# Performance work log

Hardware: AMD Instinct MI355X
Metric: run time of the kernel (lower is better)

The kernel has to match this reference:

```python
import jax, jax.numpy as jnp
import numpy as np

HEADS = 8
DIM_HEAD = 64
C = 512              # in_channels == inner_dim = heads*dim_head
WIN = 7              # window size implied by rel_pos table (2*7-1 = 13)
EPS = 1e-5


def setup_inputs() -> dict:
    key = jax.random.key(0)
    ks = jax.random.split(key, 6)
    B = 2048
    inner = HEADS * DIM_HEAD
    x = jax.random.normal(ks[0], (B, C, WIN, WIN), dtype=jnp.float32)
    gamma = jnp.ones((C,), dtype=jnp.float32)
    beta = jnp.zeros((C,), dtype=jnp.float32)
    w_qkv = jax.random.normal(ks[1], (C, 3 * inner), dtype=jnp.float32) / np.sqrt(C)
    rel_table = jax.random.normal(ks[2], (2 * WIN - 1, 2 * WIN - 1, HEADS), dtype=jnp.float32)
    w_out = jax.random.normal(ks[3], (inner, C), dtype=jnp.float32) / np.sqrt(inner)
    b_out = jnp.zeros((C,), dtype=jnp.float32)
    return {"x": x, "gamma": gamma, "beta": beta, "w_qkv": w_qkv,
            "rel_table": rel_table, "w_out": w_out, "b_out": b_out}


def _rel_pos_bias(rel_table, H, W):
    # Swin-style additive bias: bias[h, i, j] = table[hi-hj+H-1, wi-wj+W-1, h]
    hh = jnp.arange(H)
    ww = jnp.arange(W)
    hi = jnp.repeat(hh, W)          # [N] row index of each flattened position
    wi = jnp.tile(ww, H)            # [N] col index
    dh = hi[:, None] - hi[None, :] + (H - 1)   # [N, N]
    dw = wi[:, None] - wi[None, :] + (W - 1)   # [N, N]
    bias = rel_table[dh, dw]        # [N, N, heads]
    return jnp.transpose(bias, (2, 0, 1))      # [heads, N, N]


def reference(x, gamma, beta, w_qkv, rel_table, w_out, b_out):
    B, Cc, H, W = x.shape
    N = H * W
    shortcut = x
    xs = jnp.transpose(x.reshape(B, Cc, N), (0, 2, 1))   # [B, N, C]
    # LayerNorm over channel dim
    mu = jnp.mean(xs, axis=-1, keepdims=True)
    var = jnp.var(xs, axis=-1, keepdims=True)
    xn = (xs - mu) * jax.lax.rsqrt(var + EPS) * gamma + beta
    qkv = xn @ w_qkv                                      # [B, N, 3*inner]
    q, k, v = jnp.split(qkv, 3, axis=-1)
    def heads(t):
        return jnp.transpose(t.reshape(B, N, HEADS, DIM_HEAD), (0, 2, 1, 3))  # [B,h,N,d]
    q, k, v = heads(q), heads(k), heads(v)
    scale = DIM_HEAD ** -0.5
    dots = jnp.einsum('bhnd,bhmd->bhnm', q, k) * scale   # [B,h,N,N]
    dots = dots + _rel_pos_bias(rel_table, H, W)[None]   # add Swin-style bias
    attn = jax.nn.softmax(dots, axis=-1)
    out = jnp.einsum('bhnm,bhmd->bhnd', attn, v)         # [B,h,N,d]
    out = jnp.transpose(out, (0, 2, 1, 3)).reshape(B, N, HEADS * DIM_HEAD)
    out = out @ w_out + b_out                            # [B, N, C]
    out = jnp.transpose(out, (0, 2, 1)).reshape(B, Cc, H, W)
    return out + shortcut
```

## Files before the change

kernel.cpp:

```cpp
#include <hip/hip_runtime.h>

#define BATCH 2048
#define CH 512
#define NTOK 49
#define NHEAD 8
#define DHEAD 64

typedef __attribute__((ext_vector_type(8))) short bf16x8;
typedef __attribute__((ext_vector_type(4))) float f32x4;

__device__ __forceinline__ ushort f2bf(float f) {
  union { float f; unsigned u; } v; v.f = f;
  unsigned r = v.u + 0x7fffu + ((v.u >> 16) & 1u);
  return (ushort)(r >> 16);
}

__device__ __forceinline__ float bf2f(ushort u) {
  union { unsigned u; float f; } v; v.u = ((unsigned)u) << 16;
  return v.f;
}

#define MFMA16(a, b, c) __builtin_amdgcn_mfma_f32_16x16x32_bf16((a), (b), (c), 0, 0, 0)

#define GLOAD_LDS16(gsrc, ldst)                                                  \
  __builtin_amdgcn_global_load_lds((const __attribute__((address_space(1))) void*)(gsrc), \
                                   (__attribute__((address_space(3))) void*)(ldst), 16, 0, 0)

__global__ void prep_kernel(const float* __restrict__ w_qkv, const float* __restrict__ w_out,
                            const float* __restrict__ rel, ushort* __restrict__ wqkvB,
                            ushort* __restrict__ woutF, float* __restrict__ biasP) {
  int tid = blockIdx.x * blockDim.x + threadIdx.x;
  int stride = gridDim.x * blockDim.x;
  for (int i = tid; i < 12 * 16 * 8 * 64 * 8; i += stride) {
    int j = i & 7, lane = (i >> 3) & 63, cbs = (i >> 9) & 7, kk = (i >> 12) & 15, nb = i >> 16;
    int o = nb * 128 + cbs * 16 + (lane & 15);
    int c = kk * 32 + (lane >> 4) * 8 + j;
    wqkvB[i] = f2bf(w_qkv[c * 1536 + o]);
  }
  for (int i = tid; i < 32 * 16 * 64 * 8; i += stride) {
    int j = i & 7, lane = (i >> 3) & 63, ks = (i >> 9) & 15, cb = i >> 13;
    int o = cb * 16 + (lane & 15);
    int c = ks * 32 + (lane >> 4) * 8 + j;
    woutF[i] = f2bf(w_out[c * 512 + o]);
  }
  for (int i = tid; i < NHEAD * 64 * 64; i += stride) {
    int h = i >> 12, n = (i >> 6) & 63, m = i & 63;
    float v = -1e30f;
    if (n < NTOK && m < NTOK) {
      int dh = n / 7 - m / 7 + 6;
      int dw = n % 7 - m % 7 + 6;
      v = rel[(dh * 13 + dw) * 8 + h];
    }
    biasP[i] = v;
  }
}

__global__ __launch_bounds__(256) void ln_kernel(const float* __restrict__ x,
                                                 const float* __restrict__ gamma,
                                                 const float* __restrict__ beta,
                                                 ushort* __restrict__ xnW) {
  int b = blockIdx.x;
  int t = threadIdx.x;
  __shared__ ushort xsb[CH][NTOK];
  __shared__ float muL[64], rsL[64];
  const float4* x4 = (const float4*)(x + (size_t)b * CH * NTOK);
  for (int i4 = t; i4 < CH * NTOK / 4; i4 += 256) {
    float4 v = x4[i4];
    int lf = i4 * 4;
#pragma unroll
    for (int e = 0; e < 4; e++) {
      int idx = lf + e;
      int c = idx / NTOK, n = idx - c * NTOK;
      xsb[c][n] = f2bf(((const float*)&v)[e]);
    }
  }
  __syncthreads();
  int row = t >> 2, sub = t & 3;
  float s = 0.f, s2 = 0.f;
  if (row < NTOK) {
    for (int c = sub; c < CH; c += 4) {
      float v = bf2f(xsb[c][row]);
      s += v;
      s2 += v * v;
    }
  }
  s += __shfl_xor(s, 1);
  s += __shfl_xor(s, 2);
  s2 += __shfl_xor(s2, 1);
  s2 += __shfl_xor(s2, 2);
  if (sub == 0 && row < NTOK) {
    float m = s * (1.f / CH);
    muL[row] = m;
    rsL[row] = rsqrtf(s2 * (1.f / CH) - m * m + 1e-5f);
  }
  __syncthreads();
  ushort* dst = xnW + (size_t)b * NTOK * CH;
  for (int i = t; i < NTOK * 64; i += 256) {
    int n = i >> 6, c0 = (i & 63) * 8;
    float mu = muL[n], rs = rsL[n];
    ushort tmp[8];
#pragma unroll
    for (int j = 0; j < 8; j++) {
      int c = c0 + j;
      tmp[j] = f2bf((bf2f(xsb[c][n]) - mu) * rs * gamma[c] + beta[c]);
    }
    *(uint4*)(dst + (size_t)n * CH + c0) = *(const uint4*)tmp;
  }
}

__global__ __launch_bounds__(256, 4) void qkv_gemm(const ushort* __restrict__ xnW,
                                                   const ushort* __restrict__ wqkvB,
                                                   ushort* __restrict__ qW,
                                                   ushort* __restrict__ kW,
                                                   ushort* __restrict__ vW) {
  int bid = blockIdx.x;
  int f = (bid & 7) * 1176 + (bid >> 3);
  int mb = f / 12, nb = f - mb * 12;
  int r0 = mb * 128;
  int t = threadIdx.x, lane = t & 63, w = t >> 6;
  int wm = w >> 1, wn = w & 1;

  __shared__ __align__(16) ushort lds[16384];

  const int arow = lane & 15, g = lane >> 4;
  const ushort* wBbase = wqkvB + (size_t)nb * 16 * 4096;
  const ushort* xbase = xnW + (size_t)r0 * CH;

  int drow = t >> 3;
  int slot = t & 7;
  int gchunk = slot ^ (drow & 7);

#pragma unroll
  for (int i = 0; i < 4; i++) {
    int row = drow + i * 32;
    GLOAD_LDS16(xbase + (size_t)row * CH + gchunk * 8, lds + i * 2048 + t * 8);
  }
  __syncthreads();

  f32x4 acc[4][4];
#pragma unroll
  for (int mt = 0; mt < 4; mt++)
#pragma unroll
    for (int nt = 0; nt < 4; nt++) acc[mt][nt] = (f32x4){0.f, 0.f, 0.f, 0.f};

  int cur = 0;
  for (int stage = 0; stage < 8; ++stage) {
    if (stage < 7) {
      int nxt = cur ^ 1, kk = stage + 1;
#pragma unroll
      for (int i = 0; i < 4; i++) {
        GLOAD_LDS16(xbase + (size_t)(drow + i * 32) * CH + kk * 64 + gchunk * 8,
                    lds + nxt * 8192 + i * 2048 + t * 8);
      }
    }
    const ushort* lA = lds + cur * 8192;
#pragma unroll
    for (int ks = 0; ks < 2; ks++) {
      int kk2 = stage * 2 + ks;
      const ushort* wp = wBbase + (size_t)kk2 * 4096 + (wn * 4) * 512 + lane * 8;
      bf16x8 bfr[4];
#pragma unroll
      for (int nt = 0; nt < 4; nt++) bfr[nt] = *(const bf16x8*)(wp + nt * 512);
      bf16x8 afr[4];
#pragma unroll
      for (int mt = 0; mt < 4; mt++) {
        int row = wm * 64 + mt * 16 + arow;
        afr[mt] = *(const bf16x8*)&lA[row * 64 + ((ks * 4 + g) ^ (arow & 7)) * 8];
      }
#pragma unroll
      for (int mt = 0; mt < 4; mt++)
#pragma unroll
        for (int nt = 0; nt < 4; nt++) acc[mt][nt] = MFMA16(afr[mt], bfr[nt], acc[mt][nt]);
    }
    __syncthreads();
    cur ^= 1;
  }

  ushort(*oL)[136] = (ushort(*)[136])lds;
  int h0 = (nb & 3) * 2;
  int sct = nb >> 2;
#pragma unroll
  for (int hh = 0; hh < 2; hh++) {
    if (wm == hh) {
#pragma unroll
      for (int mt = 0; mt < 4; mt++)
#pragma unroll
        for (int nt = 0; nt < 4; nt++)
#pragma unroll
          for (int r = 0; r < 4; r++) {
            int rn = mt * 16 + 4 * g + r;
            oL[rn][wn * 64 + nt * 16 + arow] = f2bf(acc[mt][nt][r]);
          }
    }
    __syncthreads();
    if (sct < 2) {
      ushort* dst = (sct == 0 ? qW : kW);
      for (int i = t; i < 64 * 16; i += 256) {
        int rn = i >> 4, c8 = i & 15;
        int grow = r0 + hh * 64 + rn;
        int b = grow / 49, n = grow - b * 49;
        int h = h0 + (c8 >> 3);
        *(uint4*)(dst + (size_t)(b * 8 + h) * (NTOK * 64) + n * 64 + (c8 & 7) * 8) =
            *(const uint4*)&oL[rn][c8 * 8];
      }
    } else {
      for (int i = t; i < 64 * 128; i += 256) {
        int rn = i & 63, col = i >> 6;
        int grow = r0 + hh * 64 + rn;
        int b = grow / 49, n = grow - b * 49;
        int h = h0 + (col >> 6), d = col & 63;
        vW[(size_t)(b * 8 + h) * 4096 + d * 64 + n] = oL[rn][col];
      }
    }
    __syncthreads();
  }
}

__global__ __launch_bounds__(512) void attnproj(const ushort* __restrict__ qW,
                                                const ushort* __restrict__ kW,
                                                const ushort* __restrict__ vW,
                                                const float* __restrict__ biasP,
                                                const ushort* __restrict__ woutF,
                                                const float* __restrict__ b_out,
                                                const float* __restrict__ x,
                                                float* __restrict__ out) {
  int b = blockIdx.x;
  int t = threadIdx.x;
  int lane = t & 63;
  int w = t >> 6;

  __shared__ __align__(16) ushort lds[36864];
  ushort(*pl)[72] = (ushort(*)[72])(lds + w * 4608);

  const int c = lane & 15, g = lane >> 4;
  const ushort* qb = qW + (size_t)(b * 8 + w) * NTOK * 64;
  const ushort* kb = kW + (size_t)(b * 8 + w) * NTOK * 64;
  const ushort* vb = vW + (size_t)(b * 8 + w) * 64 * 64;
  const float* bp = biasP + w * 64 * 64;

  f32x4 s[4][4];
#pragma unroll
  for (int mt = 0; mt < 4; mt++)
#pragma unroll
    for (int nt = 0; nt < 4; nt++) s[mt][nt] = (f32x4){0.f, 0.f, 0.f, 0.f};
#pragma unroll
  for (int ks = 0; ks < 2; ks++) {
    bf16x8 kf[4];
#pragma unroll
    for (int nt = 0; nt < 4; nt++)
      kf[nt] = *(const bf16x8*)(kb + (size_t)(nt * 16 + c) * 64 + ks * 32 + g * 8);
#pragma unroll
    for (int mt = 0; mt < 4; mt++) {
      bf16x8 qf = *(const bf16x8*)(qb + (size_t)(mt * 16 + c) * 64 + ks * 32 + g * 8);
#pragma unroll
      for (int nt = 0; nt < 4; nt++) s[mt][nt] = MFMA16(qf, kf[nt], s[mt][nt]);
    }
  }
#pragma unroll
  for (int mt = 0; mt < 4; mt++)
#pragma unroll
    for (int nt = 0; nt < 4; nt++)
#pragma unroll
      for (int r = 0; r < 4; r++) {
        int n = mt * 16 + 4 * g + r;
        int m = nt * 16 + c;
        s[mt][nt][r] = s[mt][nt][r] * 0.125f + bp[n * 64 + m];
      }

#pragma unroll
  for (int mt = 0; mt < 4; mt++)
#pragma unroll
    for (int r = 0; r < 4; r++) {
      float mx = fmaxf(fmaxf(s[mt][0][r], s[mt][1][r]), fmaxf(s[mt][2][r], s[mt][3][r]));
      mx = fmaxf(mx, __shfl_xor(mx, 1));
      mx = fmaxf(mx, __shfl_xor(mx, 2));
      mx = fmaxf(mx, __shfl_xor(mx, 4));
      mx = fmaxf(mx, __shfl_xor(mx, 8));
      float p0 = __expf(s[mt][0][r] - mx);
      float p1 = __expf(s[mt][1][r] - mx);
      float p2 = __expf(s[mt][2][r] - mx);
      float p3 = __expf(s[mt][3][r] - mx);
      float sum = p0 + p1 + p2 + p3;
      sum += __shfl_xor(sum, 1);
      sum += __shfl_xor(sum, 2);
      sum += __shfl_xor(sum, 4);
      sum += __shfl_xor(sum, 8);
      float rinv = 1.f / sum;
      int n = mt * 16 + 4 * g + r;
      pl[n][0 * 16 + c] = f2bf(p0 * rinv);
      pl[n][1 * 16 + c] = f2bf(p1 * rinv);
      pl[n][2 * 16 + c] = f2bf(p2 * rinv);
      pl[n][3 * 16 + c] = f2bf(p3 * rinv);
    }

  f32x4 o[4][4];
#pragma unroll
  for (int mt = 0; mt < 4; mt++)
#pragma unroll
    for (int nt = 0; nt < 4; nt++) o[mt][nt] = (f32x4){0.f, 0.f, 0.f, 0.f};
#pragma unroll
  for (int ks = 0; ks < 2; ks++) {
    bf16x8 vf[4];
#pragma unroll
    for (int nt = 0; nt < 4; nt++)
      vf[nt] = *(const bf16x8*)(vb + (size_t)(nt * 16 + c) * 64 + ks * 32 + g * 8);
#pragma unroll
    for (int mt = 0; mt < 4; mt++) {
      bf16x8 pf = *(const bf16x8*)&pl[mt * 16 + c][ks * 32 + g * 8];
#pragma unroll
      for (int nt = 0; nt < 4; nt++) o[mt][nt] = MFMA16(pf, vf[nt], o[mt][nt]);
    }
  }
  __syncthreads();

  ushort(*aoL)[520] = (ushort(*)[520])lds;
#pragma unroll
  for (int mt = 0; mt < 4; mt++)
#pragma unroll
    for (int nt = 0; nt < 4; nt++)
#pragma unroll
      for (int r = 0; r < 4; r++) {
        int n = mt * 16 + 4 * g + r;
        aoL[n][w * 64 + nt * 16 + c] = (n < NTOK) ? f2bf(o[mt][nt][r]) : (ushort)0;
      }
  __syncthreads();

  f32x4 pacc[4][4];
#pragma unroll
  for (int mt = 0; mt < 4; mt++)
#pragma unroll
    for (int nt = 0; nt < 4; nt++) pacc[mt][nt] = (f32x4){0.f, 0.f, 0.f, 0.f};
#pragma unroll 4
  for (int step = 0; step < 16; step++) {
    bf16x8 bfr[4];
#pragma unroll
    for (int nt = 0; nt < 4; nt++)
      bfr[nt] = *(const bf16x8*)(woutF + ((size_t)((w * 4 + nt) * 16 + step)) * 512 + lane * 8);
    bf16x8 afr[4];
#pragma unroll
    for (int mt = 0; mt < 4; mt++)
      afr[mt] = *(const bf16x8*)&aoL[mt * 16 + c][step * 32 + g * 8];
#pragma unroll
    for (int mt = 0; mt < 4; mt++)
#pragma unroll
      for (int nt = 0; nt < 4; nt++) pacc[mt][nt] = MFMA16(afr[mt], bfr[nt], pacc[mt][nt]);
  }

  float(*oL)[260] = (float(*)[260])lds;
  for (int half = 0; half < 2; half++) {
    __syncthreads();
    if ((w >> 2) == half) {
      int wl = w & 3;
#pragma unroll
      for (int mt = 0; mt < 4; mt++)
#pragma unroll
        for (int nt = 0; nt < 4; nt++)
#pragma unroll
          for (int r = 0; r < 4; r++) {
            int rn = mt * 16 + 4 * g + r;
            if (rn < NTOK) oL[rn][wl * 64 + nt * 16 + c] = pacc[mt][nt][r];
          }
    }
    __syncthreads();
    int c0 = half * 256;
    const float4* x4 = (const float4*)(x + ((size_t)b * CH + c0) * NTOK);
    float4* o4 = (float4*)(out + ((size_t)b * CH + c0) * NTOK);
    const float* bo = b_out + c0;
    for (int i = t; i < 3136; i += 512) {
      float4 xv = x4[i];
      float4 ov;
      int lf = i * 4;
#pragma unroll
      for (int e = 0; e < 4; e++) {
        int cl = (lf + e) / NTOK, n = (lf + e) - cl * NTOK;
        ((float*)&ov)[e] = oL[n][cl] + bo[cl] + ((const float*)&xv)[e];
      }
      o4[i] = ov;
    }
  }
}

extern "C" void kernel_launch(void* const* d_in, const int* in_sizes, int n_in,
                              void* d_out, int out_size, void* d_ws, size_t ws_size,
                              hipStream_t stream) {
  const float* x = (const float*)d_in[0];
  const float* gamma = (const float*)d_in[1];
  const float* beta = (const float*)d_in[2];
  const float* w_qkv = (const float*)d_in[3];
  const float* rel = (const float*)d_in[4];
  const float* w_out = (const float*)d_in[5];
  const float* b_out = (const float*)d_in[6];
  float* out = (float*)d_out;

  char* ws = (char*)d_ws;
  size_t off = 0;
  ushort* wqkvB = (ushort*)(ws + off); off += (size_t)12 * 16 * 4096 * 2;
  ushort* woutF = (ushort*)(ws + off); off += (size_t)512 * 512 * 2;
  float* biasP = (float*)(ws + off);   off += (size_t)NHEAD * 64 * 64 * 4;
  ushort* qW = (ushort*)(ws + off);    off += ((size_t)BATCH * 8 * NTOK * 64 + 1024) * 2;
  ushort* kW = (ushort*)(ws + off);    off += ((size_t)BATCH * 8 * NTOK * 64 + 1024) * 2;
  ushort* vW = (ushort*)(ws + off);    off += (size_t)BATCH * 8 * 64 * 64 * 2;
  ushort* xnW = (ushort*)(ws + off);   off += (size_t)BATCH * NTOK * CH * 2;
  (void)ws_size;

  prep_kernel<<<1024, 256, 0, stream>>>(w_qkv, w_out, rel, wqkvB, woutF, biasP);
  ln_kernel<<<BATCH, 256, 0, stream>>>(x, gamma, beta, xnW);
  qkv_gemm<<<784 * 12, 256, 0, stream>>>(xnW, wqkvB, qW, kW, vW);
  attnproj<<<BATCH, 512, 0, stream>>>(qW, kW, vW, biasP, woutF, b_out, x, out);
}
```

Before: 589.2 us.

## Prelayout attention bias per lane, fold q scale into QKV GEMM, prefetch w_out fragments

Result: faster. 560.3 us (-4.9%).

```diff
diff --git a/kernel.cpp b/kernel.cpp
--- a/kernel.cpp
+++ b/kernel.cpp
@@ -28,7 +28,7 @@
 
 __global__ void prep_kernel(const float* __restrict__ w_qkv, const float* __restrict__ w_out,
                             const float* __restrict__ rel, ushort* __restrict__ wqkvB,
-                            ushort* __restrict__ woutF, float* __restrict__ biasP) {
+                            ushort* __restrict__ woutF, float* __restrict__ biasF) {
   int tid = blockIdx.x * blockDim.x + threadIdx.x;
   int stride = gridDim.x * blockDim.x;
   for (int i = tid; i < 12 * 16 * 8 * 64 * 8; i += stride) {
@@ -43,15 +43,23 @@
     int c = ks * 32 + (lane >> 4) * 8 + j;
     woutF[i] = f2bf(w_out[c * 512 + o]);
   }
-  for (int i = tid; i < NHEAD * 64 * 64; i += stride) {
-    int h = i >> 12, n = (i >> 6) & 63, m = i & 63;
-    float v = -1e30f;
-    if (n < NTOK && m < NTOK) {
-      int dh = n / 7 - m / 7 + 6;
-      int dw = n % 7 - m % 7 + 6;
-      v = rel[(dh * 13 + dw) * 8 + h];
-    }
-    biasP[i] = v;
+  for (int i = tid; i < NHEAD * 4 * 4 * 64; i += stride) {
+    int lane = i & 63, nt = (i >> 6) & 3, mt = (i >> 8) & 3, h = i >> 10;
+    int cc = lane & 15, g = lane >> 4;
+    float4 v;
+#pragma unroll
+    for (int r = 0; r < 4; r++) {
+      int n = mt * 16 + 4 * g + r;
+      int m = nt * 16 + cc;
+      float bv = -1e30f;
+      if (n < NTOK && m < NTOK) {
+        int dh = n / 7 - m / 7 + 6;
+        int dw = n % 7 - m % 7 + 6;
+        bv = rel[(dh * 13 + dw) * 8 + h];
+      }
+      ((float*)&v)[r] = bv;
+    }
+    ((float4*)biasF)[i] = v;
   }
 }
 
@@ -179,6 +187,7 @@
   ushort(*oL)[136] = (ushort(*)[136])lds;
   int h0 = (nb & 3) * 2;
   int sct = nb >> 2;
+  float sc = (sct == 0) ? 0.125f : 1.0f;
 #pragma unroll
   for (int hh = 0; hh < 2; hh++) {
     if (wm == hh) {
@@ -189,7 +198,7 @@
 #pragma unroll
           for (int r = 0; r < 4; r++) {
             int rn = mt * 16 + 4 * g + r;
-            oL[rn][wn * 64 + nt * 16 + arow] = f2bf(acc[mt][nt][r]);
+            oL[rn][wn * 64 + nt * 16 + arow] = f2bf(acc[mt][nt][r] * sc);
           }
     }
     __syncthreads();
@@ -219,7 +228,7 @@
 __global__ __launch_bounds__(512) void attnproj(const ushort* __restrict__ qW,
                                                 const ushort* __restrict__ kW,
                                                 const ushort* __restrict__ vW,
-                                                const float* __restrict__ biasP,
+                                                const float* __restrict__ biasF,
                                                 const ushort* __restrict__ woutF,
                                                 const float* __restrict__ b_out,
                                                 const float* __restrict__ x,
@@ -236,13 +245,14 @@
   const ushort* qb = qW + (size_t)(b * 8 + w) * NTOK * 64;
   const ushort* kb = kW + (size_t)(b * 8 + w) * NTOK * 64;
   const ushort* vb = vW + (size_t)(b * 8 + w) * 64 * 64;
-  const float* bp = biasP + w * 64 * 64;
+  const float4* bf = (const float4*)biasF + (size_t)w * 16 * 64;
 
   f32x4 s[4][4];
 #pragma unroll
   for (int mt = 0; mt < 4; mt++)
 #pragma unroll
     for (int nt = 0; nt < 4; nt++) s[mt][nt] = (f32x4){0.f, 0.f, 0.f, 0.f};
+  __builtin_amdgcn_s_setprio(1);
 #pragma unroll
   for (int ks = 0; ks < 2; ks++) {
     bf16x8 kf[4];
@@ -256,16 +266,16 @@
       for (int nt = 0; nt < 4; nt++) s[mt][nt] = MFMA16(qf, kf[nt], s[mt][nt]);
     }
   }
-#pragma unroll
-  for (int mt = 0; mt < 4; mt++)
-#pragma unroll
-    for (int nt = 0; nt < 4; nt++)
-#pragma unroll
-      for (int r = 0; r < 4; r++) {
-        int n = mt * 16 + 4 * g + r;
-        int m = nt * 16 + c;
-        s[mt][nt][r] = s[mt][nt][r] * 0.125f + bp[n * 64 + m];
-      }
+  __builtin_amdgcn_s_setprio(0);
+
+#pragma unroll
+  for (int mt = 0; mt < 4; mt++)
+#pragma unroll
+    for (int nt = 0; nt < 4; nt++) {
+      float4 bb = bf[(mt * 4 + nt) * 64 + lane];
+#pragma unroll
+      for (int r = 0; r < 4; r++) s[mt][nt][r] += ((const float*)&bb)[r];
+    }
 
 #pragma unroll
   for (int mt = 0; mt < 4; mt++)
@@ -298,6 +308,7 @@
   for (int mt = 0; mt < 4; mt++)
 #pragma unroll
     for (int nt = 0; nt < 4; nt++) o[mt][nt] = (f32x4){0.f, 0.f, 0.f, 0.f};
+  __builtin_amdgcn_s_setprio(1);
 #pragma unroll
   for (int ks = 0; ks < 2; ks++) {
     bf16x8 vf[4];
@@ -311,6 +322,13 @@
       for (int nt = 0; nt < 4; nt++) o[mt][nt] = MFMA16(pf, vf[nt], o[mt][nt]);
     }
   }
+  __builtin_amdgcn_s_setprio(0);
+
+  bf16x8 bcur[4];
+#pragma unroll
+  for (int nt = 0; nt < 4; nt++)
+    bcur[nt] = *(const bf16x8*)(woutF + ((size_t)((w * 4 + nt) * 16 + 0)) * 512 + lane * 8);
+
   __syncthreads();
 
   ushort(*aoL)[520] = (ushort(*)[520])lds;
@@ -330,20 +348,26 @@
   for (int mt = 0; mt < 4; mt++)
 #pragma unroll
     for (int nt = 0; nt < 4; nt++) pacc[mt][nt] = (f32x4){0.f, 0.f, 0.f, 0.f};
-#pragma unroll 4
+#pragma unroll
   for (int step = 0; step < 16; step++) {
-    bf16x8 bfr[4];
-#pragma unroll
-    for (int nt = 0; nt < 4; nt++)
-      bfr[nt] = *(const bf16x8*)(woutF + ((size_t)((w * 4 + nt) * 16 + step)) * 512 + lane * 8);
+    bf16x8 bnxt[4];
+    if (step < 15) {
+#pragma unroll
+      for (int nt = 0; nt < 4; nt++)
+        bnxt[nt] = *(const bf16x8*)(woutF + ((size_t)((w * 4 + nt) * 16 + step + 1)) * 512 + lane * 8);
+    }
     bf16x8 afr[4];
 #pragma unroll
     for (int mt = 0; mt < 4; mt++)
       afr[mt] = *(const bf16x8*)&aoL[mt * 16 + c][step * 32 + g * 8];
+    __builtin_amdgcn_s_setprio(1);
 #pragma unroll
     for (int mt = 0; mt < 4; mt++)
 #pragma unroll
-      for (int nt = 0; nt < 4; nt++) pacc[mt][nt] = MFMA16(afr[mt], bfr[nt], pacc[mt][nt]);
+      for (int nt = 0; nt < 4; nt++) pacc[mt][nt] = MFMA16(afr[mt], bcur[nt], pacc[mt][nt]);
+    __builtin_amdgcn_s_setprio(0);
+#pragma unroll
+    for (int nt = 0; nt < 4; nt++) bcur[nt] = bnxt[nt];
   }
 
   float(*oL)[260] = (float(*)[260])lds;
@@ -396,15 +420,15 @@
   size_t off = 0;
   ushort* wqkvB = (ushort*)(ws + off); off += (size_t)12 * 16 * 4096 * 2;
   ushort* woutF = (ushort*)(ws + off); off += (size_t)512 * 512 * 2;
-  float* biasP = (float*)(ws + off);   off += (size_t)NHEAD * 64 * 64 * 4;
+  float* biasF = (float*)(ws + off);   off += (size_t)NHEAD * 16 * 64 * 4 * 4;
   ushort* qW = (ushort*)(ws + off);    off += ((size_t)BATCH * 8 * NTOK * 64 + 1024) * 2;
   ushort* kW = (ushort*)(ws + off);    off += ((size_t)BATCH * 8 * NTOK * 64 + 1024) * 2;
   ushort* vW = (ushort*)(ws + off);    off += (size_t)BATCH * 8 * 64 * 64 * 2;
   ushort* xnW = (ushort*)(ws + off);   off += (size_t)BATCH * NTOK * CH * 2;
   (void)ws_size;
 
-  prep_kernel<<<1024, 256, 0, stream>>>(w_qkv, w_out, rel, wqkvB, woutF, biasP);
+  prep_kernel<<<1024, 256, 0, stream>>>(w_qkv, w_out, rel, wqkvB, woutF, biasF);
   ln_kernel<<<BATCH, 256, 0, stream>>>(x, gamma, beta, xnW);
   qkv_gemm<<<784 * 12, 256, 0, stream>>>(xnW, wqkvB, qW, kW, vW);
-  attnproj<<<BATCH, 512, 0, stream>>>(qW, kW, vW, biasP, woutF, b_out, x, out);
-}
+  attnproj<<<BATCH, 512, 0, stream>>>(qW, kW, vW, biasF, woutF, b_out, x, out);
+}
```
